# Optimization experiments

Measured on AMD Instinct MI355X. Metric: run time of the kernel, lower is better.

## Reference

```python
import jax, jax.numpy as jnp
import numpy as np

NEG_SLOPE = 0.2  # PyG GATConv default


def gat_layer(x, src, dst, W, att_src, att_dst, bias, num_nodes):
    """One PyG-style GATConv (concat=True, add_self_loops handled by caller).
    x: [N, F_in], W: [F_in, H*C], att_src/att_dst: [H, C], bias: [H*C].
    """
    H, C = att_src.shape
    h = (x @ W).reshape(num_nodes, H, C)              # [N, H, C]
    a_src = (h * att_src).sum(-1)                     # [N, H]
    a_dst = (h * att_dst).sum(-1)                     # [N, H]
    e = jax.nn.leaky_relu(a_src[src] + a_dst[dst], NEG_SLOPE)  # [E, H]
    # segment softmax over destination neighborhoods
    m = jax.ops.segment_max(e, dst, num_segments=num_nodes)   # [N, H]
    ex = jnp.exp(e - m[dst])
    denom = jax.ops.segment_sum(ex, dst, num_segments=num_nodes)
    alpha = ex / denom[dst]                           # [E, H]
    out = jax.ops.segment_sum(alpha[:, :, None] * h[src], dst,
                              num_segments=num_nodes)  # [N, H, C]
    return out.reshape(num_nodes, H * C) + bias


def setup_inputs() -> dict:
    key = jax.random.key(0)
    ks = jax.random.split(key, 12)
    N, E, D, H = 50000, 800000, 128, 8
    C = D // H
    x = jax.random.normal(ks[0], (N, D), dtype=jnp.float32)
    edge_index = jax.random.randint(ks[1], (2, E), 0, N, dtype=jnp.int64)
    s = 0.1
    return {
        "x": x,
        "edge_index": edge_index,
        "W1": s * jax.random.normal(ks[2], (D, H * C), dtype=jnp.float32),
        "as1": s * jax.random.normal(ks[3], (H, C), dtype=jnp.float32),
        "ad1": s * jax.random.normal(ks[4], (H, C), dtype=jnp.float32),
        "b1": jnp.zeros((H * C,), dtype=jnp.float32),
        "W2": s * jax.random.normal(ks[5], (D, H * C), dtype=jnp.float32),
        "as2": s * jax.random.normal(ks[6], (H, C), dtype=jnp.float32),
        "ad2": s * jax.random.normal(ks[7], (H, C), dtype=jnp.float32),
        "b2": jnp.zeros((H * C,), dtype=jnp.float32),
    }


def reference(x, edge_index, W1, as1, ad1, b1, W2, as2, ad2, b2):
    n = x.shape[0]
    # PyG GATConv default add_self_loops=True
    loop = jnp.arange(n, dtype=edge_index.dtype)
    src = jnp.concatenate([edge_index[0], loop])
    dst = jnp.concatenate([edge_index[1], loop])
    h = jax.nn.relu(gat_layer(x, src, dst, W1, as1, ad1, b1, n))
    # dropout p=0.5 is identity in eval mode
    return gat_layer(h, src, dst, W2, as2, ad2, b2, n)
```

## Files before the change

kernel.cpp:

```cpp
#include <hip/hip_runtime.h>
#include <math.h>

#define D 128
#define H 8
#define C 16
#define NEG_SLOPE 0.2f
#define SCAN_TILE 1024

typedef unsigned short ushortT;
typedef __attribute__((ext_vector_type(8))) short short8;
typedef __attribute__((ext_vector_type(4))) float f32x4;

__device__ __forceinline__ float bf2f(unsigned short v) {
    union { unsigned int i; float f; } c;
    c.i = ((unsigned int)v) << 16;
    return c.f;
}
__device__ __forceinline__ unsigned short f2bf(float f) {
    union { float f; unsigned int i; } c;
    c.f = f;
    unsigned int lsb = (c.i >> 16) & 1u;
    c.i += 0x7fffu + lsb;
    return (unsigned short)(c.i >> 16);
}


__global__ void k_hist(const int* __restrict__ ei, int* cursor,
                       int* __restrict__ rank, int E, int n) {
    int i4 = (blockIdx.x * blockDim.x + threadIdx.x) * 4;
    if (((E & 3) == 0) && i4 + 3 < E) {
        int4 dv = *(const int4*)(ei + (size_t)E + i4);
        int4 r;
        r.x = atomicAdd(cursor + dv.x, 1);
        r.y = atomicAdd(cursor + dv.y, 1);
        r.z = atomicAdd(cursor + dv.z, 1);
        r.w = atomicAdd(cursor + dv.w, 1);
        *(int4*)(rank + i4) = r;
    } else {
        for (int k = i4; k < E && k < i4 + 4; k++)
            rank[k] = atomicAdd(cursor + ei[(size_t)E + k], 1);
    }
}


__device__ __forceinline__ int padc(int c) { return (c + 4) & ~3; }

__global__ __launch_bounds__(256) void k_scan_partial(
    const int* __restrict__ cursor, int* __restrict__ bsum, int n) {
    __shared__ int lds[256];
    int t = threadIdx.x;
    int base = blockIdx.x * SCAN_TILE + t * 4;
    int s = 0;
    if (base + 3 < n) {
        int4 v = *(const int4*)(cursor + base);
        s = padc(v.x) + padc(v.y) + padc(v.z) + padc(v.w);
    } else {
        for (int k = 0; k < 4; k++)
            if (base + k < n) s += padc(cursor[base + k]);
    }
    lds[t] = s;
    __syncthreads();
    for (int st = 128; st > 0; st >>= 1) {
        if (t < st) lds[t] += lds[t + st];
        __syncthreads();
    }
    if (t == 0) bsum[blockIdx.x] = lds[0];
}

__global__ void k_scan_bsum(int* bsum, int nb) {
    if (threadIdx.x == 0 && blockIdx.x == 0) {
        int run = 0;
        for (int i = 0; i < nb; i++) {
            int v = bsum[i];
            bsum[i] = run;
            run += v;
        }
    }
}

__global__ __launch_bounds__(256) void k_scan_final(
    const int* __restrict__ cursor, int* __restrict__ poffs,
    const int* __restrict__ bsum, int n) {
    __shared__ int lds[256];
    int t = threadIdx.x;
    int base = blockIdx.x * SCAN_TILE + t * 4;
    int v[4] = {0, 0, 0, 0};
    if (base + 3 < n) {
        int4 q = *(const int4*)(cursor + base);
        v[0] = padc(q.x); v[1] = padc(q.y); v[2] = padc(q.z); v[3] = padc(q.w);
    } else {
        for (int k = 0; k < 4; k++)
            if (base + k < n) v[k] = padc(cursor[base + k]);
    }
    int s = v[0] + v[1] + v[2] + v[3];
    lds[t] = s;
    __syncthreads();
    for (int st = 1; st < 256; st <<= 1) {
        int add = (t >= st) ? lds[t - st] : 0;
        __syncthreads();
        lds[t] += add;
        __syncthreads();
    }
    int run = bsum[blockIdx.x] + ((t == 0) ? 0 : lds[t - 1]);
    if (blockIdx.x == 0 && t == 0) poffs[0] = 0;
#pragma unroll
    for (int k = 0; k < 4; k++) {
        int i = base + k;
        if (i < n) {
            run += v[k];
            poffs[i + 1] = run;
        }
    }
}

__global__ void k_fill(const int* __restrict__ ei, const int* __restrict__ poffs,
                       const int* __restrict__ cursor, const int* __restrict__ rank,
                       int* __restrict__ csrsrc, ushortT* __restrict__ hbuf,
                       float* __restrict__ asrc, int E, int n) {
    int tid = blockIdx.x * blockDim.x + threadIdx.x;
    int E4 = (E + 3) >> 2;
    if (tid < E4) {
        int i4 = tid * 4;
        if (((E & 3) == 0) && i4 + 3 < E) {
            int4 sv = *(const int4*)(ei + i4);
            int4 dv = *(const int4*)(ei + (size_t)E + i4);
            int4 rv = *(const int4*)(rank + i4);
            csrsrc[poffs[dv.x] + rv.x] = sv.x;
            csrsrc[poffs[dv.y] + rv.y] = sv.y;
            csrsrc[poffs[dv.z] + rv.z] = sv.z;
            csrsrc[poffs[dv.w] + rv.w] = sv.w;
        } else {
            for (int k = i4; k < E && k < i4 + 4; k++)
                csrsrc[poffs[ei[(size_t)E + k]] + rank[k]] = ei[k];
        }
    } else if (tid < E4 + n) {
        int i = tid - E4;
        int base = poffs[i];
        int cnt = cursor[i];
        int pd = poffs[i + 1] - base;
        csrsrc[base + cnt] = i;
        for (int k = cnt + 1; k < pd; k++) csrsrc[base + k] = n;
    } else if (tid == E4 + n) {
        int total = poffs[n];
        for (int k = 0; k < 8; k++) csrsrc[total + k] = n;
        for (int k = 0; k < D; k++) hbuf[(size_t)n * D + k] = 0;
        for (int h = 0; h < H; h++) asrc[n * H + h] = -1e30f;
    }
}


__global__ __launch_bounds__(256) void k_wprep(
    const float* __restrict__ W1, const float* __restrict__ as1,
    const float* __restrict__ ad1, const float* __restrict__ W2,
    const float* __restrict__ as2, const float* __restrict__ ad2,
    ushortT* __restrict__ wf1_hi, ushortT* __restrict__ wf1_lo,
    ushortT* __restrict__ wf2_hi, ushortT* __restrict__ wf2_lo) {
    int b = blockIdx.x;
    const float *W, *att_s, *att_d;
    ushortT *whi, *wlo;
    int idx;
    if (b < 9) {
        W = W1; att_s = as1; att_d = ad1; whi = wf1_hi; wlo = wf1_lo;
        idx = b * 256 + threadIdx.x;
    } else {
        W = W2; att_s = as2; att_d = ad2; whi = wf2_hi; wlo = wf2_lo;
        idx = (b - 9) * 256 + threadIdx.x;
    }
    if (idx >= 4 * 9 * 64) return;
    int lane = idx & 63;
    int nt = (idx >> 6) % 9;
    int kt = idx / (9 * 64);
    int quad = lane >> 4, ncol = lane & 15;
#pragma unroll
    for (int j = 0; j < 8; j++) {
        int k = kt * 32 + quad * 8 + j;
        float v;
        if (nt < 8) {
            v = W[k * D + nt * 16 + ncol];
        } else {
            const float* att = (ncol < 8) ? att_s : att_d;
            int hd = ncol & 7;
            float s = 0.f;
            for (int c = 0; c < 16; c++)
                s += W[k * D + hd * 16 + c] * att[hd * 16 + c];
            v = s;
        }
        unsigned short hi = f2bf(v);
        unsigned short lo = f2bf(v - bf2f(hi));
        whi[idx * 8 + j] = hi;
        wlo[idx * 8 + j] = lo;
    }
}


__global__ __launch_bounds__(256) void k_gemm_att(
    const float* __restrict__ x, const ushortT* __restrict__ wf_hi,
    const ushortT* __restrict__ wf_lo, ushortT* __restrict__ hout,
    float* __restrict__ as_, float* __restrict__ ad_, int n) {
    __shared__ ushortT xs_hi[8192];
    __shared__ ushortT xs_lo[8192];
    int t = threadIdx.x;
    int wq = t >> 6, lane = t & 63;
    int row0 = blockIdx.x * 64;

#pragma unroll
    for (int i = 0; i < 8; i++) {
        int e4 = t + i * 256;
        int row = e4 >> 5;
        int c4 = e4 & 31;
        int grow = row0 + row;
        float4 v = (grow < n) ? ((const float4*)(x + (size_t)grow * D))[c4]
                              : make_float4(0.f, 0.f, 0.f, 0.f);
        int k0 = c4 * 4;
        int kt = k0 >> 5, quad = (k0 >> 3) & 3, j0 = k0 & 7;
        int base = ((kt * 4 + (row >> 4)) * 64 + ((row & 15) + 16 * quad)) * 8 + j0;
        ushort4 hv, lv;
        hv.x = f2bf(v.x); lv.x = f2bf(v.x - bf2f(hv.x));
        hv.y = f2bf(v.y); lv.y = f2bf(v.y - bf2f(hv.y));
        hv.z = f2bf(v.z); lv.z = f2bf(v.z - bf2f(hv.z));
        hv.w = f2bf(v.w); lv.w = f2bf(v.w - bf2f(hv.w));
        *(ushort4*)&xs_hi[base] = hv;
        *(ushort4*)&xs_lo[base] = lv;
    }
    __syncthreads();

    f32x4 acc[9];
#pragma unroll
    for (int nt = 0; nt < 9; nt++) acc[nt] = (f32x4){0.f, 0.f, 0.f, 0.f};

#pragma unroll
    for (int kt = 0; kt < 4; kt++) {
        short8 a_hi = *(const short8*)&xs_hi[((kt * 4 + wq) * 64 + lane) * 8];
        short8 a_lo = *(const short8*)&xs_lo[((kt * 4 + wq) * 64 + lane) * 8];
        const ushortT* bh = wf_hi + (size_t)(kt * 576 + lane) * 8;
        const ushortT* bl = wf_lo + (size_t)(kt * 576 + lane) * 8;
#pragma unroll
        for (int nt = 0; nt < 9; nt++) {
            short8 b_hi = *(const short8*)(bh + nt * 512);
            short8 b_lo = *(const short8*)(bl + nt * 512);
            acc[nt] = __builtin_amdgcn_mfma_f32_16x16x32_bf16(a_hi, b_hi, acc[nt], 0, 0, 0);
            acc[nt] = __builtin_amdgcn_mfma_f32_16x16x32_bf16(a_lo, b_hi, acc[nt], 0, 0, 0);
            acc[nt] = __builtin_amdgcn_mfma_f32_16x16x32_bf16(a_hi, b_lo, acc[nt], 0, 0, 0);
        }
    }

    int q = lane >> 4, ncol = lane & 15;
    int rbase = row0 + wq * 16 + q * 4;
#pragma unroll
    for (int nt = 0; nt < 8; nt++) {
#pragma unroll
        for (int reg = 0; reg < 4; reg++) {
            int r = rbase + reg;
            if (r < n) hout[(size_t)r * D + nt * 16 + ncol] = f2bf(acc[nt][reg]);
        }
    }
#pragma unroll
    for (int reg = 0; reg < 4; reg++) {
        int r = rbase + reg;
        if (r < n) {
            float v = acc[8][reg];
            if (ncol < 8) as_[r * H + ncol] = v;
            else          ad_[r * H + (ncol - 8)] = v;
        }
    }
}


__global__ __launch_bounds__(256) void k_aggregate(
    const ushortT* __restrict__ hbuf, const float* __restrict__ asrc,
    const float* __restrict__ adst, const int* __restrict__ csr,
    const int* __restrict__ poffs, const float* __restrict__ bias,
    float* __restrict__ out, int do_relu, int n) {
    int t = threadIdx.x;
    int d = blockIdx.x * 8 + (t >> 5);
    if (d >= n) return;
    int ll = t & 31;
    int h = ll >> 2;

    int off = poffs[d];
    int degp = poffs[d + 1] - off;
    float adh = adst[d * H + h];

    float4 acc0 = make_float4(0.f, 0.f, 0.f, 0.f);
    float4 acc1 = make_float4(0.f, 0.f, 0.f, 0.f);
    float ssum = 0.f;

    int s0 = csr[off + 0], s1 = csr[off + 1], s2 = csr[off + 2], s3 = csr[off + 3];
    for (int j = 0; j < degp; j += 4) {
        int p0 = csr[off + j + 4], p1 = csr[off + j + 5];
        int p2 = csr[off + j + 6], p3 = csr[off + j + 7];
        float e0 = asrc[s0 * H + h] + adh;
        float e1 = asrc[s1 * H + h] + adh;
        float e2 = asrc[s2 * H + h] + adh;
        float e3 = asrc[s3 * H + h] + adh;
        ushort4 u0 = *(const ushort4*)(hbuf + (size_t)s0 * D + ll * 4);
        ushort4 u1 = *(const ushort4*)(hbuf + (size_t)s1 * D + ll * 4);
        ushort4 u2 = *(const ushort4*)(hbuf + (size_t)s2 * D + ll * 4);
        ushort4 u3 = *(const ushort4*)(hbuf + (size_t)s3 * D + ll * 4);
        float w0 = __expf(e0 > 0.f ? e0 : NEG_SLOPE * e0);
        float w1 = __expf(e1 > 0.f ? e1 : NEG_SLOPE * e1);
        float w2 = __expf(e2 > 0.f ? e2 : NEG_SLOPE * e2);
        float w3 = __expf(e3 > 0.f ? e3 : NEG_SLOPE * e3);
        ssum += (w0 + w1) + (w2 + w3);
        acc0.x += w0 * bf2f(u0.x); acc0.y += w0 * bf2f(u0.y);
        acc0.z += w0 * bf2f(u0.z); acc0.w += w0 * bf2f(u0.w);
        acc1.x += w1 * bf2f(u1.x); acc1.y += w1 * bf2f(u1.y);
        acc1.z += w1 * bf2f(u1.z); acc1.w += w1 * bf2f(u1.w);
        acc0.x += w2 * bf2f(u2.x); acc0.y += w2 * bf2f(u2.y);
        acc0.z += w2 * bf2f(u2.z); acc0.w += w2 * bf2f(u2.w);
        acc1.x += w3 * bf2f(u3.x); acc1.y += w3 * bf2f(u3.y);
        acc1.z += w3 * bf2f(u3.z); acc1.w += w3 * bf2f(u3.w);
        s0 = p0; s1 = p1; s2 = p2; s3 = p3;
    }

    float inv = 1.f / ssum;
    float4 b = ((const float4*)bias)[ll];
    float4 r;
    r.x = (acc0.x + acc1.x) * inv + b.x;
    r.y = (acc0.y + acc1.y) * inv + b.y;
    r.z = (acc0.z + acc1.z) * inv + b.z;
    r.w = (acc0.w + acc1.w) * inv + b.w;
    if (do_relu) {
        r.x = fmaxf(r.x, 0.f);
        r.y = fmaxf(r.y, 0.f);
        r.z = fmaxf(r.z, 0.f);
        r.w = fmaxf(r.w, 0.f);
    }
    ((float4*)(out + (size_t)d * D))[ll] = r;
}


extern "C" void kernel_launch(void* const* d_in, const int* in_sizes, int n_in,
                              void* d_out, int out_size, void* d_ws, size_t ws_size,
                              hipStream_t stream) {
    const float* x   = (const float*)d_in[0];
    const int*   ei  = (const int*)d_in[1];
    const float* W1  = (const float*)d_in[2];
    const float* as1 = (const float*)d_in[3];
    const float* ad1 = (const float*)d_in[4];
    const float* b1  = (const float*)d_in[5];
    const float* W2  = (const float*)d_in[6];
    const float* as2 = (const float*)d_in[7];
    const float* ad2 = (const float*)d_in[8];
    const float* b2  = (const float*)d_in[9];
    float* out = (float*)d_out;

    int N = in_sizes[0] / D;
    int E = in_sizes[1] / 2;
    int nb_scan = (N + SCAN_TILE - 1) / SCAN_TILE;
    const int WFN = 4 * 9 * 64 * 8;

    ushortT* hbuf = (ushortT*)d_ws;
    float* xbuf = (float*)(hbuf + (size_t)(N + 1) * D + ((N & 1) ? D : 0));
    xbuf = (float*)(hbuf + (size_t)(N + 1) * D);
    float* asrc = xbuf + (size_t)N * D;
    float* adst = asrc + (size_t)(N + 1) * H;
    int*   poffs  = (int*)(adst + (size_t)N * H);
    int*   cursor = poffs + ((N + 1 + 3) & ~3);
    int*   bsum   = cursor + ((N + 3) & ~3);
    int*   rank   = bsum + ((nb_scan + 3) & ~3);
    int*   csrsrc = rank + ((E + 3) & ~3);
    ushortT* wf1_hi = (ushortT*)(csrsrc + ((E + 4 * N + 8 + 3) & ~3));
    ushortT* wf1_lo = wf1_hi + WFN;
    ushortT* wf2_hi = wf1_lo + WFN;
    ushortT* wf2_lo = wf2_hi + WFN;

    hipMemsetAsync(cursor, 0, (size_t)N * sizeof(int), stream);

    int nb;
    nb = ((E + 3) / 4 + 255) / 256;
    k_hist<<<nb, 256, 0, stream>>>(ei, cursor, rank, E, N);
    k_scan_partial<<<nb_scan, 256, 0, stream>>>(cursor, bsum, N);
    k_scan_bsum<<<1, 64, 0, stream>>>(bsum, nb_scan);
    k_scan_final<<<nb_scan, 256, 0, stream>>>(cursor, poffs, bsum, N);
    nb = ((E + 3) / 4 + N + 1 + 255) / 256;
    k_fill<<<nb, 256, 0, stream>>>(ei, poffs, cursor, rank, csrsrc, hbuf, asrc, E, N);

    k_wprep<<<18, 256, 0, stream>>>(W1, as1, ad1, W2, as2, ad2,
                                    wf1_hi, wf1_lo, wf2_hi, wf2_lo);

    int gb = (N + 63) / 64;
    int ab = (N + 7) / 8;
    k_gemm_att<<<gb, 256, 0, stream>>>(x, wf1_hi, wf1_lo, hbuf, asrc, adst, N);
    k_aggregate<<<ab, 256, 0, stream>>>(hbuf, asrc, adst, csrsrc, poffs, b1, xbuf, 1, N);
    k_gemm_att<<<gb, 256, 0, stream>>>(xbuf, wf2_hi, wf2_lo, hbuf, asrc, adst, N);
    k_aggregate<<<ab, 256, 0, stream>>>(hbuf, asrc, adst, csrsrc, poffs, b2, out, 0, N);
}
```

Baseline: 272.1 us.

## Pre-split activations into bf16 hi/lo MFMA layout and fuse self-loop fill into scan

Layer-1 aggregation now writes its ReLU output straight into bf16 hi/lo fragments in the MFMA operand layout. A new k_xsplit kernel does the same conversion for the input x. The GEMM then reads its A operands directly from global memory, with no LDS staging or barrier, which cuts the fp32 intermediate round trip and the per-block conversion work. Self-loop and padding entries of the CSR are now written in the scan-final kernel, so k_fill launches fewer threads. The trade-off is an extra kernel launch and uncoalesced-looking scattered short writes from the aggregate kernel.

```diff
diff --git a/kernel.cpp b/kernel.cpp
--- a/kernel.cpp
+++ b/kernel.cpp
@@ -23,6 +23,7 @@
     c.i += 0x7fffu + lsb;
     return (unsigned short)(c.i >> 16);
 }
+
 
 
 __global__ void k_hist(const int* __restrict__ ei, int* cursor,
@@ -42,7 +43,6 @@
     }
 }
 
-
 __device__ __forceinline__ int padc(int c) { return (c + 4) & ~3; }
 
 __global__ __launch_bounds__(256) void k_scan_partial(
@@ -80,19 +80,19 @@
 
 __global__ __launch_bounds__(256) void k_scan_final(
     const int* __restrict__ cursor, int* __restrict__ poffs,
-    const int* __restrict__ bsum, int n) {
+    const int* __restrict__ bsum, int* __restrict__ csrsrc, int n) {
     __shared__ int lds[256];
     int t = threadIdx.x;
     int base = blockIdx.x * SCAN_TILE + t * 4;
-    int v[4] = {0, 0, 0, 0};
+    int c[4] = {0, 0, 0, 0};
     if (base + 3 < n) {
         int4 q = *(const int4*)(cursor + base);
-        v[0] = padc(q.x); v[1] = padc(q.y); v[2] = padc(q.z); v[3] = padc(q.w);
+        c[0] = q.x; c[1] = q.y; c[2] = q.z; c[3] = q.w;
     } else {
         for (int k = 0; k < 4; k++)
-            if (base + k < n) v[k] = padc(cursor[base + k]);
-    }
-    int s = v[0] + v[1] + v[2] + v[3];
+            if (base + k < n) c[k] = cursor[base + k];
+    }
+    int s = padc(c[0]) + padc(c[1]) + padc(c[2]) + padc(c[3]);
     lds[t] = s;
     __syncthreads();
     for (int st = 1; st < 256; st <<= 1) {
@@ -107,16 +107,20 @@
     for (int k = 0; k < 4; k++) {
         int i = base + k;
         if (i < n) {
-            run += v[k];
+            int pv = padc(c[k]);
+            csrsrc[run + c[k]] = i;
+            for (int k2 = c[k] + 1; k2 < pv; k2++)
+                csrsrc[run + k2] = n;
+            run += pv;
             poffs[i + 1] = run;
         }
     }
 }
 
 __global__ void k_fill(const int* __restrict__ ei, const int* __restrict__ poffs,
-                       const int* __restrict__ cursor, const int* __restrict__ rank,
-                       int* __restrict__ csrsrc, ushortT* __restrict__ hbuf,
-                       float* __restrict__ asrc, int E, int n) {
+                       const int* __restrict__ rank, int* __restrict__ csrsrc,
+                       ushortT* __restrict__ hbuf, float* __restrict__ asrc,
+                       int E, int n) {
     int tid = blockIdx.x * blockDim.x + threadIdx.x;
     int E4 = (E + 3) >> 2;
     if (tid < E4) {
@@ -133,19 +137,42 @@
             for (int k = i4; k < E && k < i4 + 4; k++)
                 csrsrc[poffs[ei[(size_t)E + k]] + rank[k]] = ei[k];
         }
-    } else if (tid < E4 + n) {
-        int i = tid - E4;
-        int base = poffs[i];
-        int cnt = cursor[i];
-        int pd = poffs[i + 1] - base;
-        csrsrc[base + cnt] = i;
-        for (int k = cnt + 1; k < pd; k++) csrsrc[base + k] = n;
-    } else if (tid == E4 + n) {
+    } else if (tid == E4) {
         int total = poffs[n];
         for (int k = 0; k < 8; k++) csrsrc[total + k] = n;
         for (int k = 0; k < D; k++) hbuf[(size_t)n * D + k] = 0;
         for (int h = 0; h < H; h++) asrc[n * H + h] = -1e30f;
     }
+}
+
+
+__global__ __launch_bounds__(256) void k_xsplit(
+    const float* __restrict__ x, ushortT* __restrict__ xh,
+    ushortT* __restrict__ xl, int n, int nt16) {
+    int idx = blockIdx.x * 256 + threadIdx.x;
+    int r = idx >> 4;
+    if (r >= nt16 * 16) return;
+    int kb = idx & 15;
+    float4 v0 = make_float4(0.f, 0.f, 0.f, 0.f), v1 = v0;
+    if (r < n) {
+        v0 = ((const float4*)(x + (size_t)r * D + kb * 8))[0];
+        v1 = ((const float4*)(x + (size_t)r * D + kb * 8))[1];
+    }
+    int wt = r >> 4, m = r & 15, kt = kb >> 2, quad = kb & 3;
+    int base = ((wt * 4 + kt) * 64 + (m + 16 * quad)) * 8;
+    ushort4 h0, l0, h1, l1;
+    h0.x = f2bf(v0.x); l0.x = f2bf(v0.x - bf2f(h0.x));
+    h0.y = f2bf(v0.y); l0.y = f2bf(v0.y - bf2f(h0.y));
+    h0.z = f2bf(v0.z); l0.z = f2bf(v0.z - bf2f(h0.z));
+    h0.w = f2bf(v0.w); l0.w = f2bf(v0.w - bf2f(h0.w));
+    h1.x = f2bf(v1.x); l1.x = f2bf(v1.x - bf2f(h1.x));
+    h1.y = f2bf(v1.y); l1.y = f2bf(v1.y - bf2f(h1.y));
+    h1.z = f2bf(v1.z); l1.z = f2bf(v1.z - bf2f(h1.z));
+    h1.w = f2bf(v1.w); l1.w = f2bf(v1.w - bf2f(h1.w));
+    *(ushort4*)(xh + base) = h0;
+    *(ushort4*)(xh + base + 4) = h1;
+    *(ushort4*)(xl + base) = l0;
+    *(ushort4*)(xl + base + 4) = l1;
 }
 
 
@@ -194,35 +221,14 @@
 
 
 __global__ __launch_bounds__(256) void k_gemm_att(
-    const float* __restrict__ x, const ushortT* __restrict__ wf_hi,
-    const ushortT* __restrict__ wf_lo, ushortT* __restrict__ hout,
-    float* __restrict__ as_, float* __restrict__ ad_, int n) {
-    __shared__ ushortT xs_hi[8192];
-    __shared__ ushortT xs_lo[8192];
+    const ushortT* __restrict__ xh, const ushortT* __restrict__ xl,
+    const ushortT* __restrict__ wf_hi, const ushortT* __restrict__ wf_lo,
+    ushortT* __restrict__ hout, float* __restrict__ as_,
+    float* __restrict__ ad_, int n) {
     int t = threadIdx.x;
-    int wq = t >> 6, lane = t & 63;
-    int row0 = blockIdx.x * 64;
-
-#pragma unroll
-    for (int i = 0; i < 8; i++) {
-        int e4 = t + i * 256;
-        int row = e4 >> 5;
-        int c4 = e4 & 31;
-        int grow = row0 + row;
-        float4 v = (grow < n) ? ((const float4*)(x + (size_t)grow * D))[c4]
-                              : make_float4(0.f, 0.f, 0.f, 0.f);
-        int k0 = c4 * 4;
-        int kt = k0 >> 5, quad = (k0 >> 3) & 3, j0 = k0 & 7;
-        int base = ((kt * 4 + (row >> 4)) * 64 + ((row & 15) + 16 * quad)) * 8 + j0;
-        ushort4 hv, lv;
-        hv.x = f2bf(v.x); lv.x = f2bf(v.x - bf2f(hv.x));
-        hv.y = f2bf(v.y); lv.y = f2bf(v.y - bf2f(hv.y));
-        hv.z = f2bf(v.z); lv.z = f2bf(v.z - bf2f(hv.z));
-        hv.w = f2bf(v.w); lv.w = f2bf(v.w - bf2f(hv.w));
-        *(ushort4*)&xs_hi[base] = hv;
-        *(ushort4*)&xs_lo[base] = lv;
-    }
-    __syncthreads();
+    int wt = blockIdx.x * 4 + (t >> 6);
+    if (wt * 16 >= n) return;
+    int lane = t & 63;
 
     f32x4 acc[9];
 #pragma unroll
@@ -230,8 +236,9 @@
 
 #pragma unroll
     for (int kt = 0; kt < 4; kt++) {
-        short8 a_hi = *(const short8*)&xs_hi[((kt * 4 + wq) * 64 + lane) * 8];
-        short8 a_lo = *(const short8*)&xs_lo[((kt * 4 + wq) * 64 + lane) * 8];
+        const ushortT* ax = xh + (size_t)((wt * 4 + kt) * 64 + lane) * 8;
+        short8 a_hi = *(const short8*)ax;
+        short8 a_lo = *(const short8*)(xl + (size_t)((wt * 4 + kt) * 64 + lane) * 8);
         const ushortT* bh = wf_hi + (size_t)(kt * 576 + lane) * 8;
         const ushortT* bl = wf_lo + (size_t)(kt * 576 + lane) * 8;
 #pragma unroll
@@ -245,7 +252,7 @@
     }
 
     int q = lane >> 4, ncol = lane & 15;
-    int rbase = row0 + wq * 16 + q * 4;
+    int rbase = wt * 16 + q * 4;
 #pragma unroll
     for (int nt = 0; nt < 8; nt++) {
 #pragma unroll
@@ -270,7 +277,8 @@
     const ushortT* __restrict__ hbuf, const float* __restrict__ asrc,
     const float* __restrict__ adst, const int* __restrict__ csr,
     const int* __restrict__ poffs, const float* __restrict__ bias,
-    float* __restrict__ out, int do_relu, int n) {
+    float* __restrict__ out, ushortT* __restrict__ oh, ushortT* __restrict__ ol,
+    int out_mode, int n) {
     int t = threadIdx.x;
     int d = blockIdx.x * 8 + (t >> 5);
     if (d >= n) return;
@@ -320,13 +328,25 @@
     r.y = (acc0.y + acc1.y) * inv + b.y;
     r.z = (acc0.z + acc1.z) * inv + b.z;
     r.w = (acc0.w + acc1.w) * inv + b.w;
-    if (do_relu) {
+
+    if (out_mode == 0) {
+        ((float4*)(out + (size_t)d * D))[ll] = r;
+    } else {
         r.x = fmaxf(r.x, 0.f);
         r.y = fmaxf(r.y, 0.f);
         r.z = fmaxf(r.z, 0.f);
         r.w = fmaxf(r.w, 0.f);
-    }
-    ((float4*)(out + (size_t)d * D))[ll] = r;
+        int wt = d >> 4, m = d & 15;
+        int kt = ll >> 3, quad = (ll >> 1) & 3, j0 = (ll & 1) * 4;
+        int base = ((wt * 4 + kt) * 64 + (m + 16 * quad)) * 8 + j0;
+        ushort4 hv, lv;
+        hv.x = f2bf(r.x); lv.x = f2bf(r.x - bf2f(hv.x));
+        hv.y = f2bf(r.y); lv.y = f2bf(r.y - bf2f(hv.y));
+        hv.z = f2bf(r.z); lv.z = f2bf(r.z - bf2f(hv.z));
+        hv.w = f2bf(r.w); lv.w = f2bf(r.w - bf2f(hv.w));
+        *(ushort4*)(oh + base) = hv;
+        *(ushort4*)(ol + base) = lv;
+    }
 }
 
 
@@ -347,13 +367,15 @@
 
     int N = in_sizes[0] / D;
     int E = in_sizes[1] / 2;
+    int NT16 = (N + 15) / 16;
     int nb_scan = (N + SCAN_TILE - 1) / SCAN_TILE;
     const int WFN = 4 * 9 * 64 * 8;
+    size_t XS = (size_t)NT16 * 2048;
 
     ushortT* hbuf = (ushortT*)d_ws;
-    float* xbuf = (float*)(hbuf + (size_t)(N + 1) * D + ((N & 1) ? D : 0));
-    xbuf = (float*)(hbuf + (size_t)(N + 1) * D);
-    float* asrc = xbuf + (size_t)N * D;
+    ushortT* xsh  = hbuf + (size_t)(N + 1) * D;
+    ushortT* xsl  = xsh + XS;
+    float* asrc = (float*)(xsl + XS);
     float* adst = asrc + (size_t)(N + 1) * H;
     int*   poffs  = (int*)(adst + (size_t)N * H);
     int*   cursor = poffs + ((N + 1 + 3) & ~3);
@@ -372,17 +394,20 @@
     k_hist<<<nb, 256, 0, stream>>>(ei, cursor, rank, E, N);
     k_scan_partial<<<nb_scan, 256, 0, stream>>>(cursor, bsum, N);
     k_scan_bsum<<<1, 64, 0, stream>>>(bsum, nb_scan);
-    k_scan_final<<<nb_scan, 256, 0, stream>>>(cursor, poffs, bsum, N);
-    nb = ((E + 3) / 4 + N + 1 + 255) / 256;
-    k_fill<<<nb, 256, 0, stream>>>(ei, poffs, cursor, rank, csrsrc, hbuf, asrc, E, N);
+    k_scan_final<<<nb_scan, 256, 0, stream>>>(cursor, poffs, bsum, csrsrc, N);
+    nb = ((E + 3) / 4 + 1 + 255) / 256;
+    k_fill<<<nb, 256, 0, stream>>>(ei, poffs, rank, csrsrc, hbuf, asrc, E, N);
 
     k_wprep<<<18, 256, 0, stream>>>(W1, as1, ad1, W2, as2, ad2,
                                     wf1_hi, wf1_lo, wf2_hi, wf2_lo);
-
-    int gb = (N + 63) / 64;
+    k_xsplit<<<NT16, 256, 0, stream>>>(x, xsh, xsl, N, NT16);
+
+    int gb = (NT16 + 3) / 4;
     int ab = (N + 7) / 8;
-    k_gemm_att<<<gb, 256, 0, stream>>>(x, wf1_hi, wf1_lo, hbuf, asrc, adst, N);
-    k_aggregate<<<ab, 256, 0, stream>>>(hbuf, asrc, adst, csrsrc, poffs, b1, xbuf, 1, N);
-    k_gemm_att<<<gb, 256, 0, stream>>>(xbuf, wf2_hi, wf2_lo, hbuf, asrc, adst, N);
-    k_aggregate<<<ab, 256, 0, stream>>>(hbuf, asrc, adst, csrsrc, poffs, b2, out, 0, N);
-}
+    k_gemm_att<<<gb, 256, 0, stream>>>(xsh, xsl, wf1_hi, wf1_lo, hbuf, asrc, adst, N);
+    k_aggregate<<<ab, 256, 0, stream>>>(hbuf, asrc, adst, csrsrc, poffs, b1,
+                                        out, xsh, xsl, 1, N);
+    k_gemm_att<<<gb, 256, 0, stream>>>(xsh, xsl, wf2_hi, wf2_lo, hbuf, asrc, adst, N);
+    k_aggregate<<<ab, 256, 0, stream>>>(hbuf, asrc, adst, csrsrc, poffs, b2,
+                                        out, xsh, xsl, 0, N);
+}
```

Measured after the change: 277.7 us. 1.02x slower.
